# Optimization experiments

Hardware: AMD Instinct MI355X
Metric: run time of the kernel (lower is better)

## Reference

```python
import jax, jax.numpy as jnp
import numpy as np

B, T, IN, H, OUT = 1024, 512, 16, 64, 8


def setup_inputs() -> dict:
    key = jax.random.key(0)
    ks = jax.random.split(key, 7)
    s = 1.0 / np.sqrt(H)
    return {
        "x": jax.random.normal(ks[0], (B, T, IN), dtype=jnp.float32),
        "W_ih": jax.random.normal(ks[1], (4 * H, IN), dtype=jnp.float32) * s,
        "W_hh": jax.random.normal(ks[2], (4 * H, H), dtype=jnp.float32) * s,
        "b_ih": jax.random.normal(ks[3], (4 * H,), dtype=jnp.float32) * s,
        "b_hh": jax.random.normal(ks[4], (4 * H,), dtype=jnp.float32) * s,
        "W_fc": jax.random.normal(ks[5], (OUT, H), dtype=jnp.float32) * s,
        "b_fc": jax.random.normal(ks[6], (OUT,), dtype=jnp.float32) * s,
    }


def reference(x, W_ih, W_hh, b_ih, b_hh, W_fc, b_fc):
    Bq, Tq, _ = x.shape
    Hq = W_hh.shape[1]
    # Precompute input contribution for all timesteps: [T, B, 4H]
    xw = jnp.einsum("bti,gi->tbg", x, W_ih) + b_ih + b_hh

    def step(carry, xw_t):
        h, c = carry
        gates = xw_t + h @ W_hh.T  # [B, 4H]
        i, f, g, o = jnp.split(gates, 4, axis=-1)  # PyTorch gate order i,f,g,o
        i = jax.nn.sigmoid(i)
        f = jax.nn.sigmoid(f)
        g = jnp.tanh(g)
        o = jax.nn.sigmoid(o)
        c = f * c + i * g
        h = o * jnp.tanh(c)
        return (h, c), None

    h0 = jnp.zeros((Bq, Hq), dtype=x.dtype)
    c0 = jnp.zeros((Bq, Hq), dtype=x.dtype)
    (h_last, _), _ = jax.lax.scan(step, (h0, c0), xw)

    # fc on last timestep only, then sigmoid -> [B, 1, OUT]
    out = jax.nn.sigmoid(h_last @ W_fc.T + b_fc)
    return out[:, None, :]
```

## Files before the change

kernel.cpp:

```cpp
#include <hip/hip_runtime.h>
#include <math.h>


#define LSTM_T 512
#define LSTM_IN 16
#define LSTM_H 64
#define LSTM_OUT 8
#define BT 4
#define HSTRIDE 72

#define L2E   1.44269504088896340736f
#define L2E2  2.88539008177792681472f

typedef _Float16 half8  __attribute__((ext_vector_type(8)));
typedef float    floatx4 __attribute__((ext_vector_type(4)));

static __device__ __forceinline__ float fast_rcp(float x) { return __builtin_amdgcn_rcpf(x); }
static __device__ __forceinline__ float fast_exp2(float x) { return __builtin_amdgcn_exp2f(x); }
static __device__ __forceinline__ float sigm2(float p) { return fast_rcp(1.0f + fast_exp2(-p)); }
static __device__ __forceinline__ float tanh2(float p) {
    return fmaf(-2.0f, fast_rcp(1.0f + fast_exp2(p)), 1.0f);
}
static __device__ __forceinline__ void pin4(int4& v) {
    asm volatile("" : "+v"(v.x), "+v"(v.y), "+v"(v.z), "+v"(v.w));
}
static __device__ __forceinline__ void pinf4(float4& v) {
    asm volatile("" : "+v"(v.x), "+v"(v.y), "+v"(v.z), "+v"(v.w));
}
static __device__ __forceinline__ void lite_barrier() {
    asm volatile("s_waitcnt lgkmcnt(0)\n\ts_barrier" ::: "memory");
}
static __device__ __forceinline__ unsigned pk2h(float a, float b) {
    return __builtin_bit_cast(unsigned, __builtin_amdgcn_cvt_pkrtz(a, b));
}
static __device__ __forceinline__ half8 to_h8(float4 a, float4 b) {
    uint4 u = make_uint4(pk2h(a.x, a.y), pk2h(a.z, a.w), pk2h(b.x, b.y), pk2h(b.z, b.w));
    return __builtin_bit_cast(half8, u);
}
static __device__ __forceinline__ int4 cvt8h(float4 a, float4 b, float sc) {
    float4 as = make_float4(a.x * sc, a.y * sc, a.z * sc, a.w * sc);
    float4 bs = make_float4(b.x * sc, b.y * sc, b.z * sc, b.w * sc);
    return __builtin_bit_cast(int4, to_h8(as, bs));
}
static __device__ __forceinline__ float4 ld4(const float* p) {
    return *reinterpret_cast<const float4*>(p);
}
static __device__ __forceinline__ float sel4(floatx4 v, bool r0, bool r1) {
    float lo = r0 ? v[1] : v[0];
    float hi = r0 ? v[3] : v[2];
    return r1 ? hi : lo;
}

__global__ __launch_bounds__(256, 1)
void lstm_mfma_kernel(const float* __restrict__ x,
                      const float* __restrict__ W_ih,
                      const float* __restrict__ W_hh,
                      const float* __restrict__ b_ih,
                      const float* __restrict__ b_hh,
                      const float* __restrict__ W_fc,
                      const float* __restrict__ b_fc,
                      float* __restrict__ out) {
    const int tid   = threadIdx.x;
    const int lane  = tid & 63;
    const int w     = tid >> 6;
    const int q     = lane >> 4;
    const int m     = lane & 15;
    const int b     = m & 3;
    const int rho   = m >> 2;
    const bool r0   = (rho & 1) != 0;
    const bool r1   = (rho & 2) != 0;
    const int jmine = 16 * w + 4 * q + rho;
    const int bbase = blockIdx.x * BT;

    __shared__ __align__(16) _Float16 hbuf[2][BT][HSTRIDE];
    __shared__ __align__(16) float hfin[BT][LSTM_H];

    int4 Ah[4][2], Ax[4];
    float4 bias4[4];
    #pragma unroll
    for (int tt = 0; tt < 4; ++tt) {
        const float sc = (tt == 2) ? L2E2 : L2E;
        const int gt = tt * 64 + 16 * w + m;
        #pragma unroll
        for (int c = 0; c < 2; ++c) {
            const float* s = W_hh + gt * LSTM_H + 32 * c + 8 * q;
            Ah[tt][c] = cvt8h(ld4(s), ld4(s + 4), sc);
            pin4(Ah[tt][c]);
        }
        float4 xa = make_float4(0.f, 0.f, 0.f, 0.f), xb = xa;
        if (q < 2) {
            const float* s = W_ih + gt * LSTM_IN + 8 * q;
            xa = ld4(s); xb = ld4(s + 4);
        }
        Ax[tt] = cvt8h(xa, xb, sc);
        pin4(Ax[tt]);
        const int gb = tt * 64 + 16 * w + 4 * q;
        float4 bi = ld4(b_ih + gb), bh = ld4(b_hh + gb);
        bias4[tt] = make_float4((bi.x + bh.x) * sc, (bi.y + bh.y) * sc,
                                (bi.z + bh.z) * sc, (bi.w + bh.w) * sc);
        pinf4(bias4[tt]);
    }

    if (tid < 128) {
        int bb = tid >> 5, jj = tid & 31;
        reinterpret_cast<int*>(&hbuf[0][bb][0])[jj] = 0;
    }

    const float* xp = x + (size_t)(bbase + b) * LSTM_T * LSTM_IN + 8 * q;
    float4 xA0 = make_float4(0.f, 0.f, 0.f, 0.f), xA1 = xA0;
    float4 xB0 = xA0, xB1 = xA0;
    if (q < 2) {
        xA0 = ld4(xp);              xA1 = ld4(xp + 4);
        xB0 = ld4(xp + LSTM_IN);    xB1 = ld4(xp + LSTM_IN + 4);
    }
    __syncthreads();

    float creg = 0.0f, hreg = 0.0f;

#define STEP(T_, X0, X1)                                                        \
    {                                                                           \
        const _Float16* cur = &hbuf[(T_) & 1][0][0];                            \
        _Float16*       nxt = &hbuf[((T_) + 1) & 1][0][0];                      \
                                         \
        half8 bh0 = *reinterpret_cast<const half8*>(cur + b * HSTRIDE + 8 * q); \
        half8 bh1 = *reinterpret_cast<const half8*>(cur + b * HSTRIDE + 32 + 8 * q); \
         \
        half8 xf = to_h8(X0, X1);                                               \
        floatx4 acc[4];                                                         \
        _Pragma("unroll")                                                       \
        for (int tt = 0; tt < 4; ++tt)                                          \
            acc[tt] = __builtin_amdgcn_mfma_f32_16x16x32_f16(                   \
                __builtin_bit_cast(half8, Ax[tt]), xf,                          \
                __builtin_bit_cast(floatx4, bias4[tt]), 0, 0, 0);               \
                       \
        if (q < 2 && (T_) + 2 < LSTM_T) {                                       \
            X0 = ld4(xp + (size_t)((T_) + 2) * LSTM_IN);                        \
            X1 = ld4(xp + (size_t)((T_) + 2) * LSTM_IN + 4);                    \
        }                                                                       \
        _Pragma("unroll")                                                       \
        for (int tt = 0; tt < 4; ++tt)                                          \
            acc[tt] = __builtin_amdgcn_mfma_f32_16x16x32_f16(                   \
                __builtin_bit_cast(half8, Ah[tt][0]), bh0, acc[tt], 0, 0, 0);   \
        _Pragma("unroll")                                                       \
        for (int tt = 0; tt < 4; ++tt)                                          \
            acc[tt] = __builtin_amdgcn_mfma_f32_16x16x32_f16(                   \
                __builtin_bit_cast(half8, Ah[tt][1]), bh1, acc[tt], 0, 0, 0);   \
               \
        float gi = sigm2(sel4(acc[0], r0, r1));                                 \
        float gf = sigm2(sel4(acc[1], r0, r1));                                 \
        float gg = tanh2(sel4(acc[2], r0, r1));                                 \
        float go = sigm2(sel4(acc[3], r0, r1));                                 \
        creg = fmaf(gf, creg, gi * gg);                                         \
        hreg = go * tanh2(creg * L2E2);                                         \
                  \
        nxt[b * HSTRIDE + jmine] = (_Float16)hreg;                              \
        lite_barrier();                                                         \
    }

    for (int t = 0; t < LSTM_T; t += 2) {
        STEP(t,     xA0, xA1)
        STEP(t + 1, xB0, xB1)
    }
#undef STEP

    hfin[b][jmine] = hreg;
    __syncthreads();

    if (tid < BT * LSTM_OUT) {
        int bb = tid >> 3, o = tid & 7;
        float s = b_fc[o];
        #pragma unroll
        for (int j4 = 0; j4 < LSTM_H / 4; ++j4) {
            float4 wv = ld4(W_fc + o * LSTM_H + 4 * j4);
            float4 hv = *reinterpret_cast<const float4*>(&hfin[bb][4 * j4]);
            s = fmaf(wv.x, hv.x, s);
            s = fmaf(wv.y, hv.y, s);
            s = fmaf(wv.z, hv.z, s);
            s = fmaf(wv.w, hv.w, s);
        }
        out[(size_t)(bbase + bb) * LSTM_OUT + o] = sigm2(s * L2E);
    }
}

extern "C" void kernel_launch(void* const* d_in, const int* in_sizes, int n_in,
                              void* d_out, int out_size, void* d_ws, size_t ws_size,
                              hipStream_t stream) {
    const float* x    = (const float*)d_in[0];
    const float* W_ih = (const float*)d_in[1];
    const float* W_hh = (const float*)d_in[2];
    const float* b_ih = (const float*)d_in[3];
    const float* b_hh = (const float*)d_in[4];
    const float* W_fc = (const float*)d_in[5];
    const float* b_fc = (const float*)d_in[6];
    float* out = (float*)d_out;

    lstm_mfma_kernel<<<1024 / BT, 256, 0, stream>>>(
        x, W_ih, W_hh, b_ih, b_hh, W_fc, b_fc, out);
}
```

Measured before the change: 267.5 us.

## Split batch lanes into two MFMA streams and hoist input projection off critical path

Each lane now handles two batch rows, b0 and b1, with rho taken from bits 1-2 of the lane index. The recurrent MFMAs run as two independent accumulator chains per step, and the input-projection MFMA for the next step is issued after the activations. This moves the x·W_ih MFMA off the serial dependency chain and gives two independent chains to interleave. The cost is that half the lanes do redundant duplicate work and skip the store (wr mask), and the recurrent MFMA count per step doubles.

```diff
diff --git a/kernel.cpp b/kernel.cpp
--- a/kernel.cpp
+++ b/kernel.cpp
@@ -65,11 +65,13 @@
     const int w     = tid >> 6;
     const int q     = lane >> 4;
     const int m     = lane & 15;
-    const int b     = m & 3;
-    const int rho   = m >> 2;
+    const int b0    = m & 1;
+    const int b1    = 2 + (m & 1);
+    const int rho   = (m >> 1) & 3;
     const bool r0   = (rho & 1) != 0;
     const bool r1   = (rho & 2) != 0;
     const int jmine = 16 * w + 4 * q + rho;
+    const bool wr   = (m < 8);
     const int bbase = blockIdx.x * BT;
 
     __shared__ __align__(16) _Float16 hbuf[2][BT][HSTRIDE];
@@ -106,64 +108,114 @@
         reinterpret_cast<int*>(&hbuf[0][bb][0])[jj] = 0;
     }
 
-    const float* xp = x + (size_t)(bbase + b) * LSTM_T * LSTM_IN + 8 * q;
-    float4 xA0 = make_float4(0.f, 0.f, 0.f, 0.f), xA1 = xA0;
-    float4 xB0 = xA0, xB1 = xA0;
+    const float* xp0 = x + (size_t)(bbase + b0) * LSTM_T * LSTM_IN + 8 * q;
+    const float* xp1 = x + (size_t)(bbase + b1) * LSTM_T * LSTM_IN + 8 * q;
+    float4 z4 = make_float4(0.f, 0.f, 0.f, 0.f);
+    float4 xE00 = z4, xE01 = z4, xE10 = z4, xE11 = z4;
+    float4 xO00 = z4, xO01 = z4, xO10 = z4, xO11 = z4;
+    float4 x000 = z4, x001 = z4, x010 = z4, x011 = z4;
     if (q < 2) {
-        xA0 = ld4(xp);              xA1 = ld4(xp + 4);
-        xB0 = ld4(xp + LSTM_IN);    xB1 = ld4(xp + LSTM_IN + 4);
+        x000 = ld4(xp0);  x001 = ld4(xp0 + 4);
+        x010 = ld4(xp1);  x011 = ld4(xp1 + 4);
+    }
+    floatx4 accA0[4], accA1[4], accB0[4], accB1[4];
+    {
+        half8 xf0 = to_h8(x000, x001);
+        half8 xf1 = to_h8(x010, x011);
+        #pragma unroll
+        for (int tt = 0; tt < 4; ++tt) {
+            accA0[tt] = __builtin_amdgcn_mfma_f32_16x16x32_f16(
+                __builtin_bit_cast(half8, Ax[tt]), xf0,
+                __builtin_bit_cast(floatx4, bias4[tt]), 0, 0, 0);
+            accA1[tt] = __builtin_amdgcn_mfma_f32_16x16x32_f16(
+                __builtin_bit_cast(half8, Ax[tt]), xf1,
+                __builtin_bit_cast(floatx4, bias4[tt]), 0, 0, 0);
+        }
+    }
+    if (q < 2) {
+        xE00 = ld4(xp0 + LSTM_IN);      xE01 = ld4(xp0 + LSTM_IN + 4);
+        xE10 = ld4(xp1 + LSTM_IN);      xE11 = ld4(xp1 + LSTM_IN + 4);
+        xO00 = ld4(xp0 + 2 * LSTM_IN);  xO01 = ld4(xp0 + 2 * LSTM_IN + 4);
+        xO10 = ld4(xp1 + 2 * LSTM_IN);  xO11 = ld4(xp1 + 2 * LSTM_IN + 4);
     }
     __syncthreads();
 
-    float creg = 0.0f, hreg = 0.0f;
-
-#define STEP(T_, X0, X1)                                                        \
+    float creg0 = 0.f, hreg0 = 0.f, creg1 = 0.f, hreg1 = 0.f;
+
+#define ACT(AIN, CREG, HREG, BOFF)                                              \
+    {                                                                           \
+        float gi = sigm2(sel4(AIN[0], r0, r1));                                 \
+        float gf = sigm2(sel4(AIN[1], r0, r1));                                 \
+        float gg = tanh2(sel4(AIN[2], r0, r1));                                 \
+        float go = sigm2(sel4(AIN[3], r0, r1));                                 \
+        CREG = fmaf(gf, CREG, gi * gg);                                         \
+        HREG = go * tanh2(CREG * L2E2);                                         \
+        if (wr) nxt[(BOFF) * HSTRIDE + jmine] = (_Float16)HREG;                 \
+    }
+
+#define ROUND(T_, XC00, XC01, XC10, XC11, AIN0, AIN1, AOUT0, AOUT1)             \
     {                                                                           \
         const _Float16* cur = &hbuf[(T_) & 1][0][0];                            \
         _Float16*       nxt = &hbuf[((T_) + 1) & 1][0][0];                      \
-                                         \
-        half8 bh0 = *reinterpret_cast<const half8*>(cur + b * HSTRIDE + 8 * q); \
-        half8 bh1 = *reinterpret_cast<const half8*>(cur + b * HSTRIDE + 32 + 8 * q); \
-         \
-        half8 xf = to_h8(X0, X1);                                               \
-        floatx4 acc[4];                                                         \
-        _Pragma("unroll")                                                       \
-        for (int tt = 0; tt < 4; ++tt)                                          \
-            acc[tt] = __builtin_amdgcn_mfma_f32_16x16x32_f16(                   \
-                __builtin_bit_cast(half8, Ax[tt]), xf,                          \
-                __builtin_bit_cast(floatx4, bias4[tt]), 0, 0, 0);               \
-                       \
-        if (q < 2 && (T_) + 2 < LSTM_T) {                                       \
-            X0 = ld4(xp + (size_t)((T_) + 2) * LSTM_IN);                        \
-            X1 = ld4(xp + (size_t)((T_) + 2) * LSTM_IN + 4);                    \
+          \
+        half8 f00 = *reinterpret_cast<const half8*>(cur + b0 * HSTRIDE + 8 * q);      \
+        half8 f01 = *reinterpret_cast<const half8*>(cur + b0 * HSTRIDE + 32 + 8 * q); \
+        half8 f10 = *reinterpret_cast<const half8*>(cur + b1 * HSTRIDE + 8 * q);      \
+        half8 f11 = *reinterpret_cast<const half8*>(cur + b1 * HSTRIDE + 32 + 8 * q); \
+        _Pragma("unroll")                                                       \
+        for (int tt = 0; tt < 4; ++tt)                                          \
+            AIN0[tt] = __builtin_amdgcn_mfma_f32_16x16x32_f16(                  \
+                __builtin_bit_cast(half8, Ah[tt][0]), f00, AIN0[tt], 0, 0, 0);  \
+        _Pragma("unroll")                                                       \
+        for (int tt = 0; tt < 4; ++tt)                                          \
+            AIN0[tt] = __builtin_amdgcn_mfma_f32_16x16x32_f16(                  \
+                __builtin_bit_cast(half8, Ah[tt][1]), f01, AIN0[tt], 0, 0, 0);  \
+        _Pragma("unroll")                                                       \
+        for (int tt = 0; tt < 4; ++tt)                                          \
+            AIN1[tt] = __builtin_amdgcn_mfma_f32_16x16x32_f16(                  \
+                __builtin_bit_cast(half8, Ah[tt][0]), f10, AIN1[tt], 0, 0, 0);  \
+        _Pragma("unroll")                                                       \
+        for (int tt = 0; tt < 4; ++tt)                                          \
+            AIN1[tt] = __builtin_amdgcn_mfma_f32_16x16x32_f16(                  \
+                __builtin_bit_cast(half8, Ah[tt][1]), f11, AIN1[tt], 0, 0, 0);  \
+           \
+        ACT(AIN0, creg0, hreg0, b0)                                             \
+        ACT(AIN1, creg1, hreg1, b1)                                             \
+                \
+        {                                                                       \
+            half8 xf0 = to_h8(XC00, XC01);                                      \
+            half8 xf1 = to_h8(XC10, XC11);                                      \
+            _Pragma("unroll")                                                   \
+            for (int tt = 0; tt < 4; ++tt) {                                    \
+                AOUT0[tt] = __builtin_amdgcn_mfma_f32_16x16x32_f16(             \
+                    __builtin_bit_cast(half8, Ax[tt]), xf0,                     \
+                    __builtin_bit_cast(floatx4, bias4[tt]), 0, 0, 0);           \
+                AOUT1[tt] = __builtin_amdgcn_mfma_f32_16x16x32_f16(             \
+                    __builtin_bit_cast(half8, Ax[tt]), xf1,                     \
+                    __builtin_bit_cast(floatx4, bias4[tt]), 0, 0, 0);           \
+            }                                                                   \
         }                                                                       \
-        _Pragma("unroll")                                                       \
-        for (int tt = 0; tt < 4; ++tt)                                          \
-            acc[tt] = __builtin_amdgcn_mfma_f32_16x16x32_f16(                   \
-                __builtin_bit_cast(half8, Ah[tt][0]), bh0, acc[tt], 0, 0, 0);   \
-        _Pragma("unroll")                                                       \
-        for (int tt = 0; tt < 4; ++tt)                                          \
-            acc[tt] = __builtin_amdgcn_mfma_f32_16x16x32_f16(                   \
-                __builtin_bit_cast(half8, Ah[tt][1]), bh1, acc[tt], 0, 0, 0);   \
-               \
-        float gi = sigm2(sel4(acc[0], r0, r1));                                 \
-        float gf = sigm2(sel4(acc[1], r0, r1));                                 \
-        float gg = tanh2(sel4(acc[2], r0, r1));                                 \
-        float go = sigm2(sel4(acc[3], r0, r1));                                 \
-        creg = fmaf(gf, creg, gi * gg);                                         \
-        hreg = go * tanh2(creg * L2E2);                                         \
-                  \
-        nxt[b * HSTRIDE + jmine] = (_Float16)hreg;                              \
+                    \
+        if (q < 2 && (T_) + 3 < LSTM_T) {                                       \
+            XC00 = ld4(xp0 + (size_t)((T_) + 3) * LSTM_IN);                     \
+            XC01 = ld4(xp0 + (size_t)((T_) + 3) * LSTM_IN + 4);                 \
+            XC10 = ld4(xp1 + (size_t)((T_) + 3) * LSTM_IN);                     \
+            XC11 = ld4(xp1 + (size_t)((T_) + 3) * LSTM_IN + 4);                 \
+        }                                                                       \
         lite_barrier();                                                         \
     }
 
     for (int t = 0; t < LSTM_T; t += 2) {
-        STEP(t,     xA0, xA1)
-        STEP(t + 1, xB0, xB1)
-    }
-#undef STEP
-
-    hfin[b][jmine] = hreg;
+        ROUND(t,     xE00, xE01, xE10, xE11, accA0, accA1, accB0, accB1)
+        ROUND(t + 1, xO00, xO01, xO10, xO11, accB0, accB1, accA0, accA1)
+    }
+#undef ROUND
+#undef ACT
+
+    if (wr) {
+        hfin[b0][jmine] = hreg0;
+        hfin[b1][jmine] = hreg1;
+    }
     __syncthreads();
 
     if (tid < BT * LSTM_OUT) {
```

Result: slower. 348.9 us (+30.4%).

## Split batch tile into two interleaved streams to overlap MFMA with activations

Applied to the files above, without the earlier changes.

Splits the four batch rows of each block into two independent pairs and interleaves their recurrence. While one pair runs its recurrent MFMAs, the other pair computes gate activations and issues the next step's input-projection MFMA. This is meant to hide MFMA latency and activation latency behind each other on the serial critical path. The cost is twice as many barriers per timestep, duplicated lanes where half of them redundantly compute values they never write (only m<8 write), and a more complex prologue and epilogue.

```diff
diff --git a/kernel.cpp b/kernel.cpp
--- a/kernel.cpp
+++ b/kernel.cpp
@@ -65,18 +65,19 @@
     const int w     = tid >> 6;
     const int q     = lane >> 4;
     const int m     = lane & 15;
-    const int b     = m & 3;
-    const int rho   = m >> 2;
+    const int b     = m & 1;
+    const int rho   = (m >> 1) & 3;
     const bool r0   = (rho & 1) != 0;
     const bool r1   = (rho & 2) != 0;
     const int jmine = 16 * w + 4 * q + rho;
+    const bool wr8  = (m < 8);
     const int bbase = blockIdx.x * BT;
 
     __shared__ __align__(16) _Float16 hbuf[2][BT][HSTRIDE];
     __shared__ __align__(16) float hfin[BT][LSTM_H];
 
     int4 Ah[4][2], Ax[4];
-    float4 bias4[4];
+    floatx4 biasC[4];
     #pragma unroll
     for (int tt = 0; tt < 4; ++tt) {
         const float sc = (tt == 2) ? L2E2 : L2E;
@@ -96,74 +97,124 @@
         pin4(Ax[tt]);
         const int gb = tt * 64 + 16 * w + 4 * q;
         float4 bi = ld4(b_ih + gb), bh = ld4(b_hh + gb);
-        bias4[tt] = make_float4((bi.x + bh.x) * sc, (bi.y + bh.y) * sc,
+        float4 bs = make_float4((bi.x + bh.x) * sc, (bi.y + bh.y) * sc,
                                 (bi.z + bh.z) * sc, (bi.w + bh.w) * sc);
-        pinf4(bias4[tt]);
+        pinf4(bs);
+        biasC[tt] = __builtin_bit_cast(floatx4, bs);
     }
 
     if (tid < 128) {
-        int bb = tid >> 5, jj = tid & 31;
-        reinterpret_cast<int*>(&hbuf[0][bb][0])[jj] = 0;
-    }
-
-    const float* xp = x + (size_t)(bbase + b) * LSTM_T * LSTM_IN + 8 * q;
-    float4 xA0 = make_float4(0.f, 0.f, 0.f, 0.f), xA1 = xA0;
-    float4 xB0 = xA0, xB1 = xA0;
+        int rr = tid >> 5, jj = tid & 31;
+        reinterpret_cast<int*>(&hbuf[1][rr][0])[jj] = 0;
+    }
+
+    const float* xp0 = x + (size_t)(bbase + 0 + b) * LSTM_T * LSTM_IN + 8 * q;
+    const float* xp1 = x + (size_t)(bbase + 2 + b) * LSTM_T * LSTM_IN + 8 * q;
+    float4 z4 = make_float4(0.f, 0.f, 0.f, 0.f);
+    float4 t00 = z4, t01 = z4, t10 = z4, t11 = z4;
+    float4 xE00 = z4, xE01 = z4, xO00 = z4, xO01 = z4;
+    float4 xE10 = z4, xE11 = z4, xO10 = z4, xO11 = z4;
     if (q < 2) {
-        xA0 = ld4(xp);              xA1 = ld4(xp + 4);
-        xB0 = ld4(xp + LSTM_IN);    xB1 = ld4(xp + LSTM_IN + 4);
-    }
+        t00 = ld4(xp0);  t01 = ld4(xp0 + 4);
+        t10 = ld4(xp1);  t11 = ld4(xp1 + 4);
+        xE00 = ld4(xp0 + LSTM_IN);      xE01 = ld4(xp0 + LSTM_IN + 4);
+        xE10 = ld4(xp1 + LSTM_IN);      xE11 = ld4(xp1 + LSTM_IN + 4);
+        xO00 = ld4(xp0 + 2 * LSTM_IN);  xO01 = ld4(xp0 + 2 * LSTM_IN + 4);
+        xO10 = ld4(xp1 + 2 * LSTM_IN);  xO11 = ld4(xp1 + 2 * LSTM_IN + 4);
+    }
+
+    floatx4 acc0[4], acc1[4];
+    {
+        half8 xf0 = to_h8(t00, t01);
+        half8 xf1 = to_h8(t10, t11);
+        #pragma unroll
+        for (int tt = 0; tt < 4; ++tt) {
+            acc0[tt] = __builtin_amdgcn_mfma_f32_16x16x32_f16(
+                __builtin_bit_cast(half8, Ax[tt]), xf0, biasC[tt], 0, 0, 0);
+            acc1[tt] = __builtin_amdgcn_mfma_f32_16x16x32_f16(
+                __builtin_bit_cast(half8, Ax[tt]), xf1, biasC[tt], 0, 0, 0);
+        }
+    }
+    float creg0 = 0.f, hreg0 = 0.f, creg1 = 0.f, hreg1 = 0.f;
     __syncthreads();
 
-    float creg = 0.0f, hreg = 0.0f;
-
-#define STEP(T_, X0, X1)                                                        \
+#define MFMA_S(S, T_, ACC)                                                      \
     {                                                                           \
-        const _Float16* cur = &hbuf[(T_) & 1][0][0];                            \
-        _Float16*       nxt = &hbuf[((T_) + 1) & 1][0][0];                      \
-                                         \
-        half8 bh0 = *reinterpret_cast<const half8*>(cur + b * HSTRIDE + 8 * q); \
-        half8 bh1 = *reinterpret_cast<const half8*>(cur + b * HSTRIDE + 32 + 8 * q); \
-         \
-        half8 xf = to_h8(X0, X1);                                               \
-        floatx4 acc[4];                                                         \
+        const _Float16* cur = &hbuf[((T_) + 1) & 1][0][0];                      \
+        half8 f0 = *reinterpret_cast<const half8*>(cur + (2*(S) + b) * HSTRIDE + 8 * q);      \
+        half8 f1 = *reinterpret_cast<const half8*>(cur + (2*(S) + b) * HSTRIDE + 32 + 8 * q); \
         _Pragma("unroll")                                                       \
         for (int tt = 0; tt < 4; ++tt)                                          \
-            acc[tt] = __builtin_amdgcn_mfma_f32_16x16x32_f16(                   \
-                __builtin_bit_cast(half8, Ax[tt]), xf,                          \
-                __builtin_bit_cast(floatx4, bias4[tt]), 0, 0, 0);               \
-                       \
-        if (q < 2 && (T_) + 2 < LSTM_T) {                                       \
-            X0 = ld4(xp + (size_t)((T_) + 2) * LSTM_IN);                        \
-            X1 = ld4(xp + (size_t)((T_) + 2) * LSTM_IN + 4);                    \
-        }                                                                       \
+            ACC[tt] = __builtin_amdgcn_mfma_f32_16x16x32_f16(                   \
+                __builtin_bit_cast(half8, Ah[tt][0]), f0, ACC[tt], 0, 0, 0);    \
         _Pragma("unroll")                                                       \
         for (int tt = 0; tt < 4; ++tt)                                          \
-            acc[tt] = __builtin_amdgcn_mfma_f32_16x16x32_f16(                   \
-                __builtin_bit_cast(half8, Ah[tt][0]), bh0, acc[tt], 0, 0, 0);   \
+            ACC[tt] = __builtin_amdgcn_mfma_f32_16x16x32_f16(                   \
+                __builtin_bit_cast(half8, Ah[tt][1]), f1, ACC[tt], 0, 0, 0);    \
+    }
+
+#define ACT_S(S, T_, ACC, XP, X0, X1, CREG, HREG)                               \
+    {                                                                           \
+        _Float16* nxt = &hbuf[(T_) & 1][0][0];                                  \
+        float gi = sigm2(sel4(ACC[0], r0, r1));                                 \
+        float gf = sigm2(sel4(ACC[1], r0, r1));                                 \
+        float gg = tanh2(sel4(ACC[2], r0, r1));                                 \
+        float go = sigm2(sel4(ACC[3], r0, r1));                                 \
+        CREG = fmaf(gf, CREG, gi * gg);                                         \
+        HREG = go * tanh2(CREG * L2E2);                                         \
+        if (wr8) nxt[(2*(S) + b) * HSTRIDE + jmine] = (_Float16)HREG;           \
+        half8 xf = to_h8(X0, X1);                                               \
         _Pragma("unroll")                                                       \
         for (int tt = 0; tt < 4; ++tt)                                          \
-            acc[tt] = __builtin_amdgcn_mfma_f32_16x16x32_f16(                   \
-                __builtin_bit_cast(half8, Ah[tt][1]), bh1, acc[tt], 0, 0, 0);   \
-               \
-        float gi = sigm2(sel4(acc[0], r0, r1));                                 \
-        float gf = sigm2(sel4(acc[1], r0, r1));                                 \
-        float gg = tanh2(sel4(acc[2], r0, r1));                                 \
-        float go = sigm2(sel4(acc[3], r0, r1));                                 \
-        creg = fmaf(gf, creg, gi * gg);                                         \
-        hreg = go * tanh2(creg * L2E2);                                         \
-                  \
-        nxt[b * HSTRIDE + jmine] = (_Float16)hreg;                              \
-        lite_barrier();                                                         \
-    }
-
-    for (int t = 0; t < LSTM_T; t += 2) {
-        STEP(t,     xA0, xA1)
-        STEP(t + 1, xB0, xB1)
-    }
-#undef STEP
-
-    hfin[b][jmine] = hreg;
+            ACC[tt] = __builtin_amdgcn_mfma_f32_16x16x32_f16(                   \
+                __builtin_bit_cast(half8, Ax[tt]), xf, biasC[tt], 0, 0, 0);     \
+        if (q < 2 && (T_) + 3 < LSTM_T) {                                       \
+            X0 = ld4(XP + (size_t)((T_) + 3) * LSTM_IN);                        \
+            X1 = ld4(XP + (size_t)((T_) + 3) * LSTM_IN + 4);                    \
+        }                                                                       \
+    }
+
+    MFMA_S(0, 0, acc0)
+    lite_barrier();
+
+    for (int t = 0; t < LSTM_T - 2; t += 2) {
+        MFMA_S(1, t, acc1)
+        ACT_S(0, t, acc0, xp0, xE00, xE01, creg0, hreg0)
+        lite_barrier();
+        MFMA_S(0, t + 1, acc0)
+        ACT_S(1, t, acc1, xp1, xE10, xE11, creg1, hreg1)
+        lite_barrier();
+        MFMA_S(1, t + 1, acc1)
+        ACT_S(0, t + 1, acc0, xp0, xO00, xO01, creg0, hreg0)
+        lite_barrier();
+        MFMA_S(0, t + 2, acc0)
+        ACT_S(1, t + 1, acc1, xp1, xO10, xO11, creg1, hreg1)
+        lite_barrier();
+    }
+    MFMA_S(1, LSTM_T - 2, acc1)
+    ACT_S(0, LSTM_T - 2, acc0, xp0, xE00, xE01, creg0, hreg0)
+    lite_barrier();
+    MFMA_S(0, LSTM_T - 1, acc0)
+    ACT_S(1, LSTM_T - 2, acc1, xp1, xE10, xE11, creg1, hreg1)
+    lite_barrier();
+    MFMA_S(1, LSTM_T - 1, acc1)
+    ACT_S(0, LSTM_T - 1, acc0, xp0, xO00, xO01, creg0, hreg0)
+    lite_barrier();
+    {
+        float gi = sigm2(sel4(acc1[0], r0, r1));
+        float gf = sigm2(sel4(acc1[1], r0, r1));
+        float gg = tanh2(sel4(acc1[2], r0, r1));
+        float go = sigm2(sel4(acc1[3], r0, r1));
+        creg1 = fmaf(gf, creg1, gi * gg);
+        hreg1 = go * tanh2(creg1 * L2E2);
+    }
+#undef MFMA_S
+#undef ACT_S
+
+    if (wr8) {
+        hfin[0 + b][jmine] = hreg0;
+        hfin[2 + b][jmine] = hreg1;
+    }
     __syncthreads();
 
     if (tid < BT * LSTM_OUT) {
```

After: 388.7 us. +45.3%, slower.
